# Optimization experiments

Measured on AMD Instinct MI355X. Metric: run time of the kernel, lower is better.

## Reference

```python
import jax, jax.numpy as jnp
import numpy as np

B, C, IMG, P, D, HEADS, L, DFF, NCLS = 32, 3, 384, 16, 512, 4, 6, 2048, 10
DH = D // HEADS          # 128
X = IMG // P             # 24 tokens per side
T = X * X                # 576 patch tokens
EPS = 1e-5               # torch LayerNorm default


def setup_inputs() -> dict:
    key = jax.random.key(0)
    ks = jax.random.split(key, 10)
    s = 0.02
    return {
        "img": jax.random.normal(ks[0], (B, C, IMG, IMG), jnp.float32),
        "Wpatch": jax.random.normal(ks[1], (C * P * P, D), jnp.float32) * s,
        "bpatch": jnp.zeros((D,), jnp.float32),
        "cls_token": jax.random.normal(ks[2], (1, 1, D), jnp.float32),
        "pos_emb": jax.random.normal(ks[3], (T + 1, D), jnp.float32),
        # per-layer params stacked on leading axis L for lax.scan
        "Wqkv": jax.random.normal(ks[4], (L, D, 3 * D), jnp.float32) * s,
        "W0": jax.random.normal(ks[5], (L, D, D), jnp.float32) * s,
        "g1": jnp.ones((L, D), jnp.float32), "b1": jnp.zeros((L, D), jnp.float32),
        "g2": jnp.ones((L, D), jnp.float32), "b2": jnp.zeros((L, D), jnp.float32),
        "W1": jax.random.normal(ks[6], (L, D, DFF), jnp.float32) * s,
        "bb1": jnp.zeros((L, DFF), jnp.float32),
        "W2": jax.random.normal(ks[7], (L, DFF, D), jnp.float32) * s,
        "bb2": jnp.zeros((L, D), jnp.float32),
        "Whead": jax.random.normal(ks[8], (D, NCLS), jnp.float32) * s,
        "bhead": jnp.zeros((NCLS,), jnp.float32),
    }


def _ln(x, g, b):
    m = x.mean(-1, keepdims=True)
    v = ((x - m) ** 2).mean(-1, keepdims=True)
    return (x - m) * jax.lax.rsqrt(v + EPS) * g + b


def _vit(img, Wpatch, bpatch, cls_token, pos_emb, Wqkv, W0,
         g1, b1, g2, b2, W1, bb1, W2, bb2, Whead, bhead):
    bsz = img.shape[0]
    # faithful rearrange 'b c (px x)(py y) -> b (x y)(px py c)' (strided patches)
    pat = img.reshape(bsz, C, P, X, P, X)            # (b, c, px, x, py, y)
    pat = pat.transpose(0, 3, 5, 2, 4, 1)            # (b, x, y, px, py, c)
    pat = pat.reshape(bsz, T, P * P * C)
    tok = pat @ Wpatch + bpatch                      # [b, T, D]
    tok = jnp.concatenate([jnp.broadcast_to(cls_token, (bsz, 1, D)), tok], axis=1)
    tok = tok + pos_emb[: T + 1]
    scale = DH ** -0.5

    def block(x, p):
        wqkv, w0, gg1, bg1, gg2, bg2, w1, c1, w2, c2 = p
        bt, tt, _ = x.shape
        # rearrange 'b t (d k h) -> k b h t d' with k=3
        qkv = (x @ wqkv).reshape(bt, tt, DH, 3, HEADS)
        q = qkv[..., 0, :].transpose(0, 3, 1, 2)     # [b, h, t, dh]
        k = qkv[..., 1, :].transpose(0, 3, 1, 2)
        v = qkv[..., 2, :].transpose(0, 3, 1, 2)
        attn = jax.nn.softmax(jnp.einsum('bhid,bhjd->bhij', q, k) * scale, axis=-1)
        o = jnp.einsum('bhij,bhjd->bhid', attn, v)
        o = o.transpose(0, 2, 1, 3).reshape(bt, tt, D) @ w0
        y = _ln(o + x, gg1, bg1)                     # postnorm block
        h = jax.nn.gelu(y @ w1 + c1, approximate=False) @ w2 + c2
        return _ln(h + y, gg2, bg2), None

    params = (Wqkv, W0, g1, b1, g2, b2, W1, bb1, W2, bb2)
    out, _ = jax.lax.scan(block, tok, params)
    return out[:, 0, :] @ Whead + bhead              # [b, NCLS]


def reference(img, Wpatch, bpatch, cls_token, pos_emb, Wqkv, W0,
              g1, b1, g2, b2, W1, bb1, W2, bb2, Whead, bhead):
    return _vit(img, Wpatch, bpatch, cls_token, pos_emb, Wqkv, W0,
                g1, b1, g2, b2, W1, bb1, W2, bb2, Whead, bhead)
```

## Files before the change

### kernel.cpp

```cpp
#include <hip/hip_runtime.h>
#include <hip/hip_bf16.h>


typedef unsigned short u16;
typedef __hip_bfloat16 bf16;
typedef __bf16 bf16x8 __attribute__((ext_vector_type(8)));
typedef float f32x4 __attribute__((ext_vector_type(4)));

typedef const __attribute__((address_space(1))) void* gas_ptr;
typedef __attribute__((address_space(3))) void* las_ptr;

#define TOKENS 577
#define TPAD   640
#define DMODEL 512
#define SM_SCALE 0.08838834764831845f
#define LAYER_W 3145728l

static __device__ __forceinline__ u16 f2b(float v) {
    bf16 t = __float2bfloat16(v);
    return *(u16*)&t;
}

template<int OUTMODE, bool GELU>
__global__ __launch_bounds__(256)
void gemm_bt(const u16* __restrict__ A, int lda,
             const u16* __restrict__ Bt, int ldb,
             float* __restrict__ Cf, bf16* __restrict__ Cb, int ldc,
             const float* __restrict__ bias, const float* __restrict__ pos,
             int K, int rows_valid)
{
    __shared__ u16 As[128 * 64];
    __shared__ u16 Bs[128 * 64];
    const int tid  = threadIdx.x;
    const int w    = tid >> 6;
    const int lane = tid & 63;
    const u16* Ab = A + (long)blockIdx.y * 128 * lda;
    const u16* Bb = Bt + (long)blockIdx.x * 128 * ldb;
    const int srow = w * 8 + (lane >> 3);
    const int scol = (lane & 7) * 8;
    const int wr = w >> 1, wc = w & 1;
    const int lr = lane & 15, lg = lane >> 4;
    f32x4 acc[4][4] = {};

    for (int kt = 0; kt < K; kt += 64) {
#pragma unroll
        for (int i = 0; i < 4; ++i) {
            const u16* ag = Ab + (long)(i * 32 + srow) * lda + kt + scol;
            const u16* bg = Bb + (long)(i * 32 + srow) * ldb + kt + scol;
            __builtin_amdgcn_global_load_lds((gas_ptr)ag, (las_ptr)&As[(i * 32 + w * 8) * 64], 16, 0, 0);
            __builtin_amdgcn_global_load_lds((gas_ptr)bg, (las_ptr)&Bs[(i * 32 + w * 8) * 64], 16, 0, 0);
        }
        __syncthreads();
#pragma unroll
        for (int kk = 0; kk < 2; ++kk) {
            const int ko = kk * 32 + lg * 8;
            bf16x8 af[4], bv[4];
#pragma unroll
            for (int m = 0; m < 4; ++m)
                af[m] = *(const bf16x8*)&As[(wr * 64 + m * 16 + lr) * 64 + ko];
#pragma unroll
            for (int n = 0; n < 4; ++n)
                bv[n] = *(const bf16x8*)&Bs[(wc * 64 + n * 16 + lr) * 64 + ko];
#pragma unroll
            for (int m = 0; m < 4; ++m)
#pragma unroll
                for (int n = 0; n < 4; ++n)
                    acc[m][n] = __builtin_amdgcn_mfma_f32_16x16x32_bf16(af[m], bv[n], acc[m][n], 0, 0, 0);
        }
        __syncthreads();
    }

    const int cbase = blockIdx.x * 128 + wc * 64;
    const int rbase = blockIdx.y * 128 + wr * 64;
#pragma unroll
    for (int n = 0; n < 4; ++n) {
        const int c = cbase + n * 16 + lr;
        const float bval = bias ? bias[c] : 0.0f;
#pragma unroll
        for (int m = 0; m < 4; ++m) {
#pragma unroll
            for (int j = 0; j < 4; ++j) {
                const int r = rbase + m * 16 + lg * 4 + j;
                if (r >= rows_valid) continue;
                float v = acc[m][n][j] + bval;
                if constexpr (GELU) v = 0.5f * v * (1.0f + erff(v * 0.70710678118654752f));
                long idx;
                if constexpr (OUTMODE == 1) {
                    const int pb = r / 576, pt = r - pb * 576;
                    v += pos[(long)(1 + pt) * DMODEL + c];
                    idx = (long)(pb * TOKENS + 1 + pt) * ldc + c;
                } else {
                    idx = (long)r * ldc + c;
                }
                if (Cf) Cf[idx] = v;
                if (Cb) Cb[idx] = __float2bfloat16(v);
            }
        }
    }
}

template<bool GELU, bool PACKED>
__global__ __launch_bounds__(256)
void gemm_bt32(const u16* __restrict__ A, int lda,
               const u16* __restrict__ Bt, int ldb,
               bf16* __restrict__ Cb, int ldc,
               const float* __restrict__ bias, int K, int rows_valid)
{
    __shared__ u16 As[128 * 32];
    __shared__ u16 Bs[128 * 32];
    const int tid  = threadIdx.x;
    const int w    = tid >> 6;
    const int lane = tid & 63;
    const u16* Ab = A + (long)blockIdx.y * 128 * lda;
    const u16* Bb = Bt + (long)blockIdx.x * 128 * ldb;
    const int wr = w >> 1, wc = w & 1;
    const int lr = lane & 15, lg = lane >> 4;
    f32x4 acc[4][4] = {};

    for (int kt = 0; kt < K; kt += 32) {
#pragma unroll
        for (int rd = 0; rd < 2; ++rd) {
            const int idx = rd * 256 + tid;
            const int row = idx >> 2, g = idx & 3;
            const int sg = g ^ ((row >> 1) & 3);
            __builtin_amdgcn_global_load_lds(
                (gas_ptr)(Ab + (long)row * lda + kt + sg * 8), (las_ptr)&As[idx * 8], 16, 0, 0);
            __builtin_amdgcn_global_load_lds(
                (gas_ptr)(Bb + (long)row * ldb + kt + sg * 8), (las_ptr)&Bs[idx * 8], 16, 0, 0);
        }
        __syncthreads();
        bf16x8 af[4], bv[4];
#pragma unroll
        for (int m = 0; m < 4; ++m) {
            const int r = wr * 64 + m * 16 + lr;
            af[m] = *(const bf16x8*)&As[r * 32 + (lg ^ ((r >> 1) & 3)) * 8];
        }
#pragma unroll
        for (int n = 0; n < 4; ++n) {
            const int r = wc * 64 + n * 16 + lr;
            bv[n] = *(const bf16x8*)&Bs[r * 32 + (lg ^ ((r >> 1) & 3)) * 8];
        }
#pragma unroll
        for (int m = 0; m < 4; ++m)
#pragma unroll
            for (int n = 0; n < 4; ++n)
                acc[m][n] = __builtin_amdgcn_mfma_f32_16x16x32_bf16(af[m], bv[n], acc[m][n], 0, 0, 0);
        __syncthreads();
    }

    const int cbase = blockIdx.x * 128 + wc * 64;
    const int rbase = blockIdx.y * 128 + wr * 64;
    float bval[4];
#pragma unroll
    for (int n = 0; n < 4; ++n) bval[n] = bias ? bias[cbase + n * 16 + lr] : 0.0f;

    if constexpr (PACKED) {
#pragma unroll
        for (int m = 0; m < 4; ++m) {
#pragma unroll
            for (int j = 0; j < 4; ++j) {
                const int r = rbase + m * 16 + lg * 4 + j;
                if (r >= rows_valid) continue;
                u16 pk[4];
#pragma unroll
                for (int n = 0; n < 4; ++n) {
                    float v = acc[m][n][j] + bval[n];
                    if constexpr (GELU) v = 0.5f * v * (1.0f + erff(v * 0.70710678118654752f));
                    pk[n] = f2b(v);
                }
                *(uint2*)&Cb[(long)r * ldc + cbase + lr * 4] = *(uint2*)pk;
            }
        }
    } else {
#pragma unroll
        for (int n = 0; n < 4; ++n) {
            const int c = cbase + n * 16 + lr;
#pragma unroll
            for (int m = 0; m < 4; ++m) {
#pragma unroll
                for (int j = 0; j < 4; ++j) {
                    const int r = rbase + m * 16 + lg * 4 + j;
                    if (r >= rows_valid) continue;
                    float v = acc[m][n][j] + bval[n];
                    if constexpr (GELU) v = 0.5f * v * (1.0f + erff(v * 0.70710678118654752f));
                    Cb[(long)r * ldc + c] = __float2bfloat16(v);
                }
            }
        }
    }
}

__global__ __launch_bounds__(512)
void proj_ln(const u16* __restrict__ A, const u16* __restrict__ Bt,
             const float* __restrict__ res,
             const float* __restrict__ g, const float* __restrict__ b,
             float* __restrict__ outf, bf16* __restrict__ outb, int Mrows)
{
    __shared__ u16 As[64 * 32];
    __shared__ u16 Bs[512 * 32];
    __shared__ float redS[4][64];
    __shared__ float redQ[4][64];
    const int tid = threadIdx.x, wid = tid >> 6, lane = tid & 63;
    const int wm = wid >> 2, wn = wid & 3;
    const int lr = lane & 15, lg = lane >> 4;
    const long row0 = (long)blockIdx.x * 64;
    const u16* Ab = A + row0 * DMODEL;
    f32x4 acc[2][8] = {};

    for (int kt = 0; kt < 512; kt += 32) {
#pragma unroll
        for (int rd = 0; rd < 4; ++rd) {
            const int idx = rd * 512 + tid;
            const int row = idx >> 2, gg = idx & 3;
            const int sg = gg ^ ((row >> 1) & 3);
            __builtin_amdgcn_global_load_lds(
                (gas_ptr)(Bt + (long)row * DMODEL + kt + sg * 8), (las_ptr)&Bs[idx * 8], 16, 0, 0);
        }
        if (tid < 256) {
            const int row = tid >> 2, gg = tid & 3;
            const int sg = gg ^ ((row >> 1) & 3);
            __builtin_amdgcn_global_load_lds(
                (gas_ptr)(Ab + (long)row * DMODEL + kt + sg * 8), (las_ptr)&As[tid * 8], 16, 0, 0);
        }
        __syncthreads();
        bf16x8 af[2], bv[8];
#pragma unroll
        for (int m = 0; m < 2; ++m) {
            const int r = wm * 32 + m * 16 + lr;
            af[m] = *(const bf16x8*)&As[r * 32 + (lg ^ ((r >> 1) & 3)) * 8];
        }
#pragma unroll
        for (int n = 0; n < 8; ++n) {
            const int r = wn * 128 + n * 16 + lr;
            bv[n] = *(const bf16x8*)&Bs[r * 32 + (lg ^ ((r >> 1) & 3)) * 8];
        }
#pragma unroll
        for (int m = 0; m < 2; ++m)
#pragma unroll
            for (int n = 0; n < 8; ++n)
                acc[m][n] = __builtin_amdgcn_mfma_f32_16x16x32_bf16(af[m], bv[n], acc[m][n], 0, 0, 0);
        __syncthreads();
    }

    float ps[2][4], pq[2][4];
#pragma unroll
    for (int m = 0; m < 2; ++m)
#pragma unroll
        for (int j = 0; j < 4; ++j) {
            const long r = row0 + wm * 32 + m * 16 + lg * 4 + j;
            const bool valid = r < Mrows;
            float s = 0.f, q = 0.f;
#pragma unroll
            for (int n = 0; n < 8; ++n) {
                float t = acc[m][n][j];
                if (valid) t += res[r * DMODEL + wn * 128 + n * 16 + lr];
                acc[m][n][j] = t;
                s += t; q += t * t;
            }
            ps[m][j] = s; pq[m][j] = q;
        }
#pragma unroll
    for (int o = 1; o < 16; o <<= 1)
#pragma unroll
        for (int m = 0; m < 2; ++m)
#pragma unroll
            for (int j = 0; j < 4; ++j) {
                ps[m][j] += __shfl_xor(ps[m][j], o);
                pq[m][j] += __shfl_xor(pq[m][j], o);
            }
    if (lr == 0) {
#pragma unroll
        for (int m = 0; m < 2; ++m)
#pragma unroll
            for (int j = 0; j < 4; ++j) {
                const int ri = wm * 32 + m * 16 + lg * 4 + j;
                redS[wn][ri] = ps[m][j];
                redQ[wn][ri] = pq[m][j];
            }
    }
    __syncthreads();
    if (tid < 64) {
        const float s = redS[0][tid] + redS[1][tid] + redS[2][tid] + redS[3][tid];
        const float q = redQ[0][tid] + redQ[1][tid] + redQ[2][tid] + redQ[3][tid];
        const float mean = s * (1.f / 512.f);
        const float var = q * (1.f / 512.f) - mean * mean;
        redS[0][tid] = mean;
        redQ[0][tid] = rsqrtf(var + 1e-5f);
    }
    __syncthreads();
#pragma unroll
    for (int m = 0; m < 2; ++m)
#pragma unroll
        for (int j = 0; j < 4; ++j) {
            const int ri = wm * 32 + m * 16 + lg * 4 + j;
            const long r = row0 + ri;
            if (r >= Mrows) continue;
            const float mean = redS[0][ri], rs = redQ[0][ri];
#pragma unroll
            for (int n = 0; n < 8; ++n) {
                const int c = wn * 128 + n * 16 + lr;
                const float o = (acc[m][n][j] - mean) * rs * g[c] + b[c];
                outf[r * DMODEL + c] = o;
                outb[r * DMODEL + c] = __float2bfloat16(o);
            }
        }
}

template<int OUTMODE, bool GELU>
__global__ __launch_bounds__(512, 1)
void gemm8(const u16* __restrict__ A, int lda,
           const u16* __restrict__ Bt, int ldb,
           float* __restrict__ Cf, bf16* __restrict__ Cb, int ldc,
           const float* __restrict__ bias, const float* __restrict__ pos,
           int K, int rows_valid)
{
    __shared__ u16 Ash[2][2][256 * 32];
    __shared__ u16 Bsh[2][2][256 * 32];
    const int tid = threadIdx.x, wid = tid >> 6, lane = tid & 63;
    const int wm = wid >> 2, wn = wid & 3;
    const int lr = lane & 15, lg = lane >> 4;
    const u16* Ab = A + (long)blockIdx.y * 256 * lda;
    const u16* Bb = Bt + (long)blockIdx.x * 256 * ldb;
    const int srow = tid >> 2;
    const int soct = ((tid & 3) ^ (srow & 3)) * 8;
    const int slot8 = (lg ^ (lr & 3)) * 8;

    f32x4 acc[8][4] = {};

    auto stage = [&](u16* dst, const u16* src, int ld, int kt, int kh) {
#pragma unroll
        for (int i = 0; i < 2; ++i)
            __builtin_amdgcn_global_load_lds(
                (gas_ptr)(src + (long)(i * 128 + srow) * ld + kt * 64 + kh * 32 + soct),
                (las_ptr)(dst + (i * 512 + tid) * 8), 16, 0, 0);
    };

#define VMW(n) { asm volatile("s_waitcnt vmcnt(" #n ")" ::: "memory"); \
                 __builtin_amdgcn_sched_barrier(0); }
#define MFMA16(A0)                                                              \
    __builtin_amdgcn_s_setprio(1);                                             \
    _Pragma("unroll")                                                           \
    for (int m = 0; m < 4; ++m)                                                 \
        _Pragma("unroll")                                                       \
        for (int n = 0; n < 4; ++n)                                             \
            acc[(A0) + m][n] = __builtin_amdgcn_mfma_f32_16x16x32_bf16(         \
                af[m], bfr[n], acc[(A0) + m][n], 0, 0, 0);                      \
    __builtin_amdgcn_s_setprio(0);

    const int nt = K / 64;
    stage(&Ash[0][0][0], Ab, lda, 0, 0);
    stage(&Bsh[0][0][0], Bb, ldb, 0, 0);
    stage(&Ash[0][1][0], Ab, lda, 0, 1);
    stage(&Bsh[0][1][0], Bb, ldb, 0, 1);
    VMW(4);
    __builtin_amdgcn_s_barrier();

    for (int t = 0; t < nt; ++t) {
        const int db = t & 1;
        const bool nx = (t + 1 < nt);
        bf16x8 af[4], bfr[4];

#pragma unroll
        for (int n = 0; n < 4; ++n)
            bfr[n] = *(const bf16x8*)&Bsh[db][0][(wn * 64 + n * 16 + lr) * 32 + slot8];
#pragma unroll
        for (int m = 0; m < 4; ++m)
            af[m] = *(const bf16x8*)&Ash[db][0][(wm * 128 + m * 16 + lr) * 32 + slot8];
        if (nx) stage(&Ash[db ^ 1][0][0], Ab, lda, t + 1, 0);
        __builtin_amdgcn_s_barrier();
        MFMA16(0)
        __builtin_amdgcn_s_barrier();

#pragma unroll
        for (int m = 0; m < 4; ++m)
            af[m] = *(const bf16x8*)&Ash[db][0][(wm * 128 + 64 + m * 16 + lr) * 32 + slot8];
        if (nx) { stage(&Bsh[db ^ 1][0][0], Bb, ldb, t + 1, 0); VMW(4); }
        else    { VMW(0); }
        __builtin_amdgcn_s_barrier();
        MFMA16(4)
        __builtin_amdgcn_s_barrier();

#pragma unroll
        for (int n = 0; n < 4; ++n)
            bfr[n] = *(const bf16x8*)&Bsh[db][1][(wn * 64 + n * 16 + lr) * 32 + slot8];
#pragma unroll
        for (int m = 0; m < 4; ++m)
            af[m] = *(const bf16x8*)&Ash[db][1][(wm * 128 + m * 16 + lr) * 32 + slot8];
        if (nx) stage(&Ash[db ^ 1][1][0], Ab, lda, t + 1, 1);
        __builtin_amdgcn_s_barrier();
        MFMA16(0)
        __builtin_amdgcn_s_barrier();

#pragma unroll
        for (int m = 0; m < 4; ++m)
            af[m] = *(const bf16x8*)&Ash[db][1][(wm * 128 + 64 + m * 16 + lr) * 32 + slot8];
        if (nx) { stage(&Bsh[db ^ 1][1][0], Bb, ldb, t + 1, 1); VMW(4); }
        __builtin_amdgcn_s_barrier();
        MFMA16(4)
        __builtin_amdgcn_s_barrier();
    }
#undef MFMA16
#undef VMW

    const int cbase = blockIdx.x * 256 + wn * 64;
    const int rbase = blockIdx.y * 256 + wm * 128;
#pragma unroll
    for (int n = 0; n < 4; ++n) {
        const int c = cbase + n * 16 + lr;
        const float bval = bias ? bias[c] : 0.0f;
#pragma unroll
        for (int a = 0; a < 8; ++a) {
#pragma unroll
            for (int j = 0; j < 4; ++j) {
                const int r = rbase + a * 16 + lg * 4 + j;
                if (r >= rows_valid) continue;
                float v = acc[a][n][j] + bval;
                if constexpr (GELU) v = 0.5f * v * (1.0f + erff(v * 0.70710678118654752f));
                long idx;
                if constexpr (OUTMODE == 1) {
                    const int pb = r / 576, pt = r - pb * 576;
                    v += pos[(long)(1 + pt) * DMODEL + c];
                    idx = (long)(pb * TOKENS + 1 + pt) * ldc + c;
                } else {
                    idx = (long)r * ldc + c;
                }
                if (Cf) Cf[idx] = v;
                if (Cb) Cb[idx] = __float2bfloat16(v);
            }
        }
    }
}

__global__ __launch_bounds__(256, 2)
void attn_flash(const u16* __restrict__ qkv, const u16* __restrict__ vhT,
                bf16* __restrict__ ob)
{
    __shared__ u16 Ksh[2][64 * 128];
    __shared__ u16 Vsh[2][128 * 64];
    __shared__ u16 Psh[128 * 64];
    const int tid = threadIdx.x;
    const int w = tid >> 6, lane = tid & 63;
    const int lr = lane & 15, lg = lane >> 4;
    const int pair = blockIdx.y;
    const int b = pair >> 2, h = pair & 3;
    const int q0 = blockIdx.x * 128;
    const long rowbase = (long)b * TOKENS;
    const int swrd = lr & 7;

    const u16* kg = qkv + rowbase * 1536 + 512 + h * 128;
    const u16* vg = vhT + (long)pair * 128 * TPAD;

    auto stageK = [&](int buf, int t) {
#pragma unroll
        for (int i = 0; i < 4; ++i) {
            const int slot = i * 256 + tid;
            const int row = slot >> 4, s = slot & 15;
            const int so = (s & 8) | ((s & 7) ^ (row & 7));
            __builtin_amdgcn_global_load_lds(
                (gas_ptr)(kg + (long)(t * 64 + row) * 1536 + so * 8),
                (las_ptr)&Ksh[buf][slot * 8], 16, 0, 0);
        }
    };
    auto stageV = [&](int buf, int t) {
#pragma unroll
        for (int i = 0; i < 4; ++i) {
            const int slot = i * 256 + tid;
            const int row = slot >> 3, s = slot & 7;
            const int so = s ^ (row & 7);
            __builtin_amdgcn_global_load_lds(
                (gas_ptr)(vg + (long)row * TPAD + t * 64 + so * 8),
                (las_ptr)&Vsh[buf][slot * 8], 16, 0, 0);
        }
    };

    bf16x8 qf[2][4];
#pragma unroll
    for (int m = 0; m < 2; ++m)
#pragma unroll
        for (int kf = 0; kf < 4; ++kf) {
            const long r = rowbase + q0 + w * 32 + m * 16 + lr;
            qf[m][kf] = *(const bf16x8*)&qkv[r * 1536 + h * 128 + kf * 32 + lg * 8];
        }

    float mrun[2][4], lrun[2][4];
#pragma unroll
    for (int m = 0; m < 2; ++m)
#pragma unroll
        for (int j = 0; j < 4; ++j) { mrun[m][j] = -1e30f; lrun[m][j] = 0.f; }
    f32x4 oacc[2][8] = {};

    constexpr int NT = TPAD / 64;
    stageK(0, 0); stageV(0, 0);
    stageK(1, 1); stageV(1, 1);
    asm volatile("s_waitcnt vmcnt(8)" ::: "memory");
    __builtin_amdgcn_sched_barrier(0);
    __builtin_amdgcn_s_barrier();

    for (int t = 0; t < NT; ++t) {
        const int cur = t & 1;

        f32x4 s[2][4] = {};
#pragma unroll
        for (int kf = 0; kf < 4; ++kf) {
            const int o = kf * 4 + lg;
            const int so = ((o & 8) | ((o & 7) ^ swrd)) * 8;
            bf16x8 bv[4];
#pragma unroll
            for (int n = 0; n < 4; ++n)
                bv[n] = *(const bf16x8*)&Ksh[cur][(n * 16 + lr) * 128 + so];
            __builtin_amdgcn_s_setprio(1);
#pragma unroll
            for (int m = 0; m < 2; ++m)
#pragma unroll
                for (int n = 0; n < 4; ++n)
                    s[m][n] = __builtin_amdgcn_mfma_f32_16x16x32_bf16(qf[m][kf], bv[n], s[m][n], 0, 0, 0);
            __builtin_amdgcn_s_setprio(0);
        }

        float sc[2][4];
#pragma unroll
        for (int m = 0; m < 2; ++m)
#pragma unroll
            for (int jj = 0; jj < 4; ++jj) {
                float mx = mrun[m][jj];
#pragma unroll
                for (int n = 0; n < 4; ++n) {
                    const int col = t * 64 + n * 16 + lr;
                    float v = s[m][n][jj] * SM_SCALE;
                    v = (col < TOKENS) ? v : -1e30f;
                    s[m][n][jj] = v;
                    mx = fmaxf(mx, v);
                }
#pragma unroll
                for (int o = 1; o < 16; o <<= 1) mx = fmaxf(mx, __shfl_xor(mx, o));
                const float f = __expf(mrun[m][jj] - mx);
                sc[m][jj] = f;
                float sum = 0.f;
#pragma unroll
                for (int n = 0; n < 4; ++n) {
                    const float p = __expf(s[m][n][jj] - mx);
                    s[m][n][jj] = p;
                    sum += p;
                }
#pragma unroll
                for (int o = 1; o < 16; o <<= 1) sum += __shfl_xor(sum, o);
                lrun[m][jj] = lrun[m][jj] * f + sum;
                mrun[m][jj] = mx;
            }
#pragma unroll
        for (int m = 0; m < 2; ++m)
#pragma unroll
            for (int n = 0; n < 8; ++n)
#pragma unroll
                for (int jj = 0; jj < 4; ++jj) oacc[m][n][jj] *= sc[m][jj];

#pragma unroll
        for (int m = 0; m < 2; ++m)
#pragma unroll
            for (int jj = 0; jj < 4; ++jj) {
                const int prow = w * 32 + m * 16 + lg * 4 + jj;
                const int p7 = prow & 7;
#pragma unroll
                for (int n = 0; n < 4; ++n) {
                    const int c = n * 16 + lr;
                    Psh[prow * 64 + (((c >> 3) ^ p7) << 3) + (c & 7)] = f2b(s[m][n][jj]);
                }
            }

#pragma unroll
        for (int kf = 0; kf < 2; ++kf) {
            const int so = ((kf * 4 + lg) ^ swrd) * 8;
            bf16x8 pa[2];
#pragma unroll
            for (int m = 0; m < 2; ++m)
                pa[m] = *(const bf16x8*)&Psh[(w * 32 + m * 16 + lr) * 64 + so];
            __builtin_amdgcn_s_setprio(1);
#pragma unroll
            for (int n = 0; n < 8; ++n) {
                const bf16x8 vb = *(const bf16x8*)&Vsh[cur][(n * 16 + lr) * 64 + so];
#pragma unroll
                for (int m = 0; m < 2; ++m)
                    oacc[m][n] = __builtin_amdgcn_mfma_f32_16x16x32_bf16(pa[m], vb, oacc[m][n], 0, 0, 0);
            }
            __builtin_amdgcn_s_setprio(0);
        }

        __builtin_amdgcn_s_barrier();
        if (t + 2 < NT) { stageK(cur, t + 2); stageV(cur, t + 2); }
        if (t + 1 < NT) {
            if (t + 2 < NT) { asm volatile("s_waitcnt vmcnt(8)" ::: "memory"); }
            else            { asm volatile("s_waitcnt vmcnt(0)" ::: "memory"); }
            __builtin_amdgcn_sched_barrier(0);
        }
        __builtin_amdgcn_s_barrier();
    }

#pragma unroll
    for (int m = 0; m < 2; ++m)
#pragma unroll
        for (int jj = 0; jj < 4; ++jj) {
            const float inv = 1.f / lrun[m][jj];
            const int q = q0 + w * 32 + m * 16 + lg * 4 + jj;
            if (q >= TOKENS) continue;
#pragma unroll
            for (int n = 0; n < 8; ++n)
                ob[(rowbase + q) * DMODEL + h * 128 + n * 16 + lr] =
                    __float2bfloat16(oacc[m][n][jj] * inv);
        }
}

__global__ __launch_bounds__(256)
void wtrans(const float* __restrict__ W, bf16* __restrict__ WT, int K, int N)
{
    __shared__ float tile[32][33];
    const int n0 = blockIdx.x * 32, k0 = blockIdx.y * 32;
    const int tx = threadIdx.x & 31, ty = threadIdx.x >> 5;
#pragma unroll
    for (int i = 0; i < 4; ++i)
        tile[ty + i * 8][tx] = W[(long)(k0 + ty + i * 8) * N + n0 + tx];
    __syncthreads();
#pragma unroll
    for (int i = 0; i < 4; ++i)
        WT[(long)(n0 + ty + i * 8) * K + k0 + tx] = __float2bfloat16(tile[tx][ty + i * 8]);
}

__global__ __launch_bounds__(256)
void wtrans_layers(const float* __restrict__ Wqkv, const float* __restrict__ W0,
                   const float* __restrict__ W1, const float* __restrict__ W2,
                   bf16* __restrict__ out, int layer0)
{
    const int bb = blockIdx.x;
    const int sl = bb / 3072;
    const int l = layer0 + sl;
    int t = bb % 3072;
    bf16* base = out + (long)sl * LAYER_W;
    const float* W; bf16* WT; int K, N; int mode = 0;
    if (t < 768)       {            W = Wqkv + (long)l * 512 * 1536; WT = base;           K = 512;  N = 1536; mode = 1; }
    else if (t < 1024) { t -= 768;  W = W0   + (long)l * 512 * 512;  WT = base + 786432;  K = 512;  N = 512;  }
    else if (t < 2048) { t -= 1024; W = W1   + (long)l * 512 * 2048; WT = base + 1048576; K = 512;  N = 2048; }
    else               { t -= 2048; W = W2   + (long)l * 2048 * 512; WT = base + 2097152; K = 2048; N = 512;  mode = 2; }
    const int nx = N / 32;
    const int n0 = (t % nx) * 32, k0 = (t / nx) * 32;
    __shared__ float tile[32][33];
    const int tx = threadIdx.x & 31, ty = threadIdx.x >> 5;
#pragma unroll
    for (int i = 0; i < 4; ++i)
        tile[ty + i * 8][tx] = W[(long)(k0 + ty + i * 8) * N + n0 + tx];
    __syncthreads();
#pragma unroll
    for (int i = 0; i < 4; ++i) {
        int n = n0 + ty + i * 8;
        if (mode == 1) {
            const int d = n / 12, rr = n % 12;
            n = (rr >> 2) * 512 + (rr & 3) * 128 + d;
        }
        int kk = k0 + tx;
        if (mode == 2) {
            const int s = kk & 63;
            kk = (kk & ~63) | (((s & 15) << 2) | (s >> 4));
        }
        WT[(long)n * K + kk] = __float2bfloat16(tile[tx][ty + i * 8]);
    }
}

__global__ __launch_bounds__(64)
void patch_gather(const float* __restrict__ img, bf16* __restrict__ pat)
{
    const int bid = blockIdx.x;
    const int x  = bid % 24;
    const int p1 = (bid / 24) % 16;
    const int b  = bid / (24 * 16);
    __shared__ bf16 lds[24][48];
    const int lane = threadIdx.x;
    const int h = p1 * 24 + x;
    for (int c = 0; c < 3; ++c) {
        const float* row = img + ((long)(b * 3 + c) * 384 + h) * 384;
#pragma unroll
        for (int i = 0; i < 6; ++i) {
            const int wpix = lane + i * 64;
            const float v = row[wpix];
            const int y = wpix % 24, p2 = wpix / 24;
            lds[y][p2 * 3 + c] = __float2bfloat16(v);
        }
    }
    __syncthreads();
    for (int idx = lane; idx < 24 * 48; idx += 64) {
        const int y = idx / 48, j = idx % 48;
        pat[(long)(b * 576 + x * 24 + y) * 768 + p1 * 48 + j] = lds[y][j];
    }
}

__global__ __launch_bounds__(256)
void clsfill(const float* __restrict__ cls, const float* __restrict__ pos,
             float* __restrict__ tokf, bf16* __restrict__ xb)
{
    const int i = blockIdx.x * 256 + threadIdx.x;
    const int b = i >> 9, d = i & 511;
    const float v = cls[d] + pos[d];
    tokf[(long)b * TOKENS * DMODEL + d] = v;
    xb[(long)b * TOKENS * DMODEL + d] = __float2bfloat16(v);
}

__global__ __launch_bounds__(256)
void repack_v(const u16* __restrict__ qkv, u16* __restrict__ vhT)
{
    __shared__ u16 lds[64][136];
    const int bid = blockIdx.x;
    const int tt = bid % 10, pair = bid / 10;
    const int b = pair >> 2, h = pair & 3;
    const int tid = threadIdx.x;
    const int tl = tid >> 2, seg = tid & 3;
    const long row = (long)b * TOKENS + tt * 64 + tl;
    const u16* src = qkv + row * 1536 + 1024 + h * 128 + seg * 32;
#pragma unroll
    for (int u = 0; u < 4; ++u)
        *(uint4*)&lds[tl][seg * 32 + u * 8] = *(const uint4*)&src[u * 8];
    __syncthreads();
    const int d = tid >> 1, th = (tid & 1) * 32;
    u16* dst = vhT + ((long)pair * 128 + d) * TPAD + tt * 64 + th;
#pragma unroll
    for (int blk = 0; blk < 4; ++blk) {
        uint4 pk; u16* pp = (u16*)&pk;
#pragma unroll
        for (int j = 0; j < 8; ++j) {
            const int t = tt * 64 + th + blk * 8 + j;
            pp[j] = (t < TOKENS) ? lds[th + blk * 8 + j][d] : (u16)0;
        }
        *(uint4*)&dst[blk * 8] = pk;
    }
}

__global__ __launch_bounds__(256)
void resln(const float* __restrict__ xin, const float* __restrict__ res,
           const float* __restrict__ g, const float* __restrict__ b,
           float* __restrict__ outf, bf16* __restrict__ outb, int nrows)
{
    const int row = blockIdx.x * 4 + (threadIdx.x >> 6);
    if (row >= nrows) return;
    const int lane = threadIdx.x & 63;
    const float* p1 = xin + (long)row * DMODEL;
    const float* p2 = res + (long)row * DMODEL;
    float v[8];
    float s = 0.f;
#pragma unroll
    for (int i = 0; i < 8; ++i) { v[i] = p1[lane + i * 64] + p2[lane + i * 64]; s += v[i]; }
#pragma unroll
    for (int o = 32; o; o >>= 1) s += __shfl_xor(s, o);
    const float mean = s * (1.f / 512.f);
    float q = 0.f;
#pragma unroll
    for (int i = 0; i < 8; ++i) { const float d = v[i] - mean; q += d * d; }
#pragma unroll
    for (int o = 32; o; o >>= 1) q += __shfl_xor(q, o);
    const float rs = rsqrtf(q * (1.f / 512.f) + 1e-5f);
#pragma unroll
    for (int i = 0; i < 8; ++i) {
        const int c = lane + i * 64;
        const float o = (v[i] - mean) * rs * g[c] + b[c];
        outf[(long)row * DMODEL + c] = o;
        outb[(long)row * DMODEL + c] = __float2bfloat16(o);
    }
}

__global__ __launch_bounds__(64)
void head_k(const float* __restrict__ tokf, const float* __restrict__ Wh,
            const float* __restrict__ bh, float* __restrict__ out)
{
    const int b = blockIdx.x;
    const int lane = threadIdx.x;
    const float* x = tokf + (long)b * TOKENS * DMODEL;
    float acc[10] = {};
#pragma unroll
    for (int i = 0; i < 8; ++i) {
        const int d = lane + i * 64;
        const float xv = x[d];
        const float* wr = Wh + (long)d * 10;
#pragma unroll
        for (int c = 0; c < 10; ++c) acc[c] += xv * wr[c];
    }
#pragma unroll
    for (int c = 0; c < 10; ++c)
#pragma unroll
        for (int o = 32; o; o >>= 1) acc[c] += __shfl_xor(acc[c], o);
    if (lane == 0) {
#pragma unroll
        for (int c = 0; c < 10; ++c) out[b * 10 + c] = acc[c] + bh[c];
    }
}

extern "C" void kernel_launch(void* const* d_in, const int* in_sizes, int n_in,
                              void* d_out, int out_size, void* d_ws, size_t ws_size,
                              hipStream_t stream)
{
    (void)in_sizes; (void)n_in; (void)out_size;
    const float* img    = (const float*)d_in[0];
    const float* Wpatch = (const float*)d_in[1];
    const float* bpatch = (const float*)d_in[2];
    const float* clstk  = (const float*)d_in[3];
    const float* pos    = (const float*)d_in[4];
    const float* Wqkv   = (const float*)d_in[5];
    const float* W0     = (const float*)d_in[6];
    const float* g1     = (const float*)d_in[7];
    const float* b1     = (const float*)d_in[8];
    const float* g2     = (const float*)d_in[9];
    const float* b2     = (const float*)d_in[10];
    const float* W1     = (const float*)d_in[11];
    const float* bb1    = (const float*)d_in[12];
    const float* W2     = (const float*)d_in[13];
    const float* bb2    = (const float*)d_in[14];
    const float* Whead  = (const float*)d_in[15];
    const float* bhead  = (const float*)d_in[16];

    static const int cand[7][2] = {{32,6},{32,1},{16,1},{8,1},{4,1},{2,1},{1,1}};
    int Bc = 0, nW = 1;
    size_t o_tokf=0, o_xb=0, o_R1=0, o_R2=0, o_ob=0, o_wp=0, o_wr=0;
    for (int ci = 0; ci < 7; ++ci) {
        const int bc = cand[ci][0], nw = cand[ci][1];
        const long Mrows = (long)bc * TOKENS;
        const long Mpad  = ((Mrows + 255) / 256) * 256;
        size_t off = 0;
        auto take = [&](size_t sz) { size_t o = off; off += (sz + 255) & ~(size_t)255; return o; };
        size_t t_tokf = take((size_t)Mpad * 512 * 4);
        size_t t_xb   = take((size_t)Mpad * 512 * 2);
        size_t t_R1   = take((size_t)Mpad * 2048 * 2);
        size_t r2a = (size_t)bc * 4 * TPAD * 128 * 2;
        size_t r2b = (size_t)Mpad * 512 * 4;
        size_t t_R2 = take(r2a > r2b ? r2a : r2b);
        size_t t_ob   = take((size_t)Mpad * 512 * 2);
        size_t t_wp   = take((size_t)512 * 768 * 2);
        size_t t_wr   = take((size_t)nw * LAYER_W * 2);
        if (off <= ws_size) {
            Bc = bc; nW = nw;
            o_tokf=t_tokf; o_xb=t_xb; o_R1=t_R1; o_R2=t_R2; o_ob=t_ob; o_wp=t_wp; o_wr=t_wr;
            break;
        }
    }
    if (Bc == 0) return;

    const long Mrows = (long)Bc * TOKENS;
    const long Mpad  = ((Mrows + 255) / 256) * 256;
    const int  NP    = Bc * 4;
    const int  gy128 = (int)(Mpad / 128);
    const int  gy256 = (int)(Mpad / 256);
    const int  nproj = (int)((Mrows + 63) / 64);
    const long patRows = ((long)Bc * 576 + 127) / 128 * 128;

    char* base = (char*)d_ws;
    float* tokf = (float*)(base + o_tokf);
    bf16*  xb   = (bf16*)(base + o_xb);
    char*  R1   = base + o_R1;
    char*  R2   = base + o_R2;
    bf16*  ob   = (bf16*)(base + o_ob);
    bf16*  wpT  = (bf16*)(base + o_wp);
    bf16*  wAll = (bf16*)(base + o_wr);

    u16*  qkvb = (u16*)R1;
    bf16* pat  = (bf16*)R1;
    u16*  h1b  = (u16*)R1;
    u16*  vhT  = (u16*)R2;
    float* t1  = (float*)R2;

    wtrans<<<dim3(512 / 32, 768 / 32), 256, 0, stream>>>(Wpatch, wpT, 768, 512);
    if (nW == 6)
        wtrans_layers<<<6 * 3072, 256, 0, stream>>>(Wqkv, W0, W1, W2, wAll, 0);

    const int nchunks = 32 / Bc;
    for (int ch = 0; ch < nchunks; ++ch) {
        const float* img_c = img + (long)ch * Bc * 3 * 384 * 384;

        hipMemsetAsync(xb, 0, (size_t)Mpad * 512 * 2, stream);
        clsfill<<<Bc * 2, 256, 0, stream>>>(clstk, pos, tokf, xb);
        patch_gather<<<Bc * 16 * 24, 64, 0, stream>>>(img_c, pat);
        gemm_bt<1, false><<<dim3(4, (int)(patRows / 128)), 256, 0, stream>>>(
            (const u16*)pat, 768, (const u16*)wpT, 768,
            tokf, xb, 512, bpatch, pos, 768, Bc * 576);

        for (int l = 0; l < 6; ++l) {
            const bf16* wL = wAll + (nW == 6 ? (long)l * LAYER_W : 0);
            if (nW == 1)
                wtrans_layers<<<3072, 256, 0, stream>>>(Wqkv, W0, W1, W2, wAll, l);
            const u16* wqkvT = (const u16*)wL;
            const u16* w0T   = (const u16*)(wL + 786432);
            const u16* w1T   = (const u16*)(wL + 1048576);
            const u16* w2T   = (const u16*)(wL + 2097152);

            gemm_bt32<false, false><<<dim3(12, gy128), 256, 0, stream>>>(
                (const u16*)xb, 512, wqkvT, 512,
                (bf16*)qkvb, 1536, nullptr, 512, (int)Mpad);

            repack_v<<<NP * 10, 256, 0, stream>>>(qkvb, vhT);
            attn_flash<<<dim3(5, NP), 256, 0, stream>>>(qkvb, vhT, ob);

            proj_ln<<<nproj, 512, 0, stream>>>(
                (const u16*)ob, w0T, tokf, g1 + l * 512, b1 + l * 512,
                tokf, xb, (int)Mrows);

            gemm_bt32<true, true><<<dim3(16, gy128), 256, 0, stream>>>(
                (const u16*)xb, 512, w1T, 512,
                (bf16*)h1b, 2048, bb1 + l * 2048, 512, (int)Mrows);

            gemm8<0, false><<<dim3(2, gy256), 512, 0, stream>>>(
                (const u16*)h1b, 2048, w2T, 2048,
                t1, nullptr, 512, bb2 + l * 512, nullptr, 2048, (int)Mrows);
            resln<<<(int)((Mrows + 3) / 4), 256, 0, stream>>>(
                t1, tokf, g2 + l * 512, b2 + l * 512, tokf, xb, (int)Mrows);
        }

        head_k<<<Bc, 64, 0, stream>>>(tokf, Whead, bhead, (float*)d_out + (long)ch * Bc * 10);
    }
}
```

Before: 2.646 ms.

## Replace custom FFN2 and patch GEMMs with shared 128-tile kernel and bf16 output

New measurement: 2.448 ms. 1.08x faster.

```diff
diff --git a/kernel.cpp b/kernel.cpp
--- a/kernel.cpp
+++ b/kernel.cpp
@@ -21,90 +21,13 @@
     return *(u16*)&t;
 }
 
-template<int OUTMODE, bool GELU>
-__global__ __launch_bounds__(256)
-void gemm_bt(const u16* __restrict__ A, int lda,
-             const u16* __restrict__ Bt, int ldb,
-             float* __restrict__ Cf, bf16* __restrict__ Cb, int ldc,
-             const float* __restrict__ bias, const float* __restrict__ pos,
-             int K, int rows_valid)
-{
-    __shared__ u16 As[128 * 64];
-    __shared__ u16 Bs[128 * 64];
-    const int tid  = threadIdx.x;
-    const int w    = tid >> 6;
-    const int lane = tid & 63;
-    const u16* Ab = A + (long)blockIdx.y * 128 * lda;
-    const u16* Bb = Bt + (long)blockIdx.x * 128 * ldb;
-    const int srow = w * 8 + (lane >> 3);
-    const int scol = (lane & 7) * 8;
-    const int wr = w >> 1, wc = w & 1;
-    const int lr = lane & 15, lg = lane >> 4;
-    f32x4 acc[4][4] = {};
-
-    for (int kt = 0; kt < K; kt += 64) {
-#pragma unroll
-        for (int i = 0; i < 4; ++i) {
-            const u16* ag = Ab + (long)(i * 32 + srow) * lda + kt + scol;
-            const u16* bg = Bb + (long)(i * 32 + srow) * ldb + kt + scol;
-            __builtin_amdgcn_global_load_lds((gas_ptr)ag, (las_ptr)&As[(i * 32 + w * 8) * 64], 16, 0, 0);
-            __builtin_amdgcn_global_load_lds((gas_ptr)bg, (las_ptr)&Bs[(i * 32 + w * 8) * 64], 16, 0, 0);
-        }
-        __syncthreads();
-#pragma unroll
-        for (int kk = 0; kk < 2; ++kk) {
-            const int ko = kk * 32 + lg * 8;
-            bf16x8 af[4], bv[4];
-#pragma unroll
-            for (int m = 0; m < 4; ++m)
-                af[m] = *(const bf16x8*)&As[(wr * 64 + m * 16 + lr) * 64 + ko];
-#pragma unroll
-            for (int n = 0; n < 4; ++n)
-                bv[n] = *(const bf16x8*)&Bs[(wc * 64 + n * 16 + lr) * 64 + ko];
-#pragma unroll
-            for (int m = 0; m < 4; ++m)
-#pragma unroll
-                for (int n = 0; n < 4; ++n)
-                    acc[m][n] = __builtin_amdgcn_mfma_f32_16x16x32_bf16(af[m], bv[n], acc[m][n], 0, 0, 0);
-        }
-        __syncthreads();
-    }
-
-    const int cbase = blockIdx.x * 128 + wc * 64;
-    const int rbase = blockIdx.y * 128 + wr * 64;
-#pragma unroll
-    for (int n = 0; n < 4; ++n) {
-        const int c = cbase + n * 16 + lr;
-        const float bval = bias ? bias[c] : 0.0f;
-#pragma unroll
-        for (int m = 0; m < 4; ++m) {
-#pragma unroll
-            for (int j = 0; j < 4; ++j) {
-                const int r = rbase + m * 16 + lg * 4 + j;
-                if (r >= rows_valid) continue;
-                float v = acc[m][n][j] + bval;
-                if constexpr (GELU) v = 0.5f * v * (1.0f + erff(v * 0.70710678118654752f));
-                long idx;
-                if constexpr (OUTMODE == 1) {
-                    const int pb = r / 576, pt = r - pb * 576;
-                    v += pos[(long)(1 + pt) * DMODEL + c];
-                    idx = (long)(pb * TOKENS + 1 + pt) * ldc + c;
-                } else {
-                    idx = (long)r * ldc + c;
-                }
-                if (Cf) Cf[idx] = v;
-                if (Cb) Cb[idx] = __float2bfloat16(v);
-            }
-        }
-    }
-}
-
-template<bool GELU, bool PACKED>
+template<bool GELU, int OMODE>
 __global__ __launch_bounds__(256)
 void gemm_bt32(const u16* __restrict__ A, int lda,
                const u16* __restrict__ Bt, int ldb,
-               bf16* __restrict__ Cb, int ldc,
-               const float* __restrict__ bias, int K, int rows_valid)
+               bf16* __restrict__ Cb, float* __restrict__ Cf, int ldc,
+               const float* __restrict__ bias, const float* __restrict__ pos,
+               int K, int rows_valid)
 {
     __shared__ u16 As[128 * 32];
     __shared__ u16 Bs[128 * 32];
@@ -154,7 +77,7 @@
 #pragma unroll
     for (int n = 0; n < 4; ++n) bval[n] = bias ? bias[cbase + n * 16 + lr] : 0.0f;
 
-    if constexpr (PACKED) {
+    if constexpr (OMODE == 1) {
 #pragma unroll
         for (int m = 0; m < 4; ++m) {
 #pragma unroll
@@ -169,6 +92,24 @@
                     pk[n] = f2b(v);
                 }
                 *(uint2*)&Cb[(long)r * ldc + cbase + lr * 4] = *(uint2*)pk;
+            }
+        }
+    } else if constexpr (OMODE == 3) {
+#pragma unroll
+        for (int m = 0; m < 4; ++m) {
+#pragma unroll
+            for (int j = 0; j < 4; ++j) {
+                const int r = rbase + m * 16 + lg * 4 + j;
+                if (r >= rows_valid) continue;
+                const int pb = r / 576, pt = r - pb * 576;
+                const long orow = (long)pb * TOKENS + 1 + pt;
+#pragma unroll
+                for (int n = 0; n < 4; ++n) {
+                    const int c = cbase + n * 16 + lr;
+                    const float v = acc[m][n][j] + bval[n] + pos[(long)(1 + pt) * DMODEL + c];
+                    Cf[orow * ldc + c] = v;
+                    Cb[orow * ldc + c] = __float2bfloat16(v);
+                }
             }
         }
     } else {
@@ -304,131 +245,6 @@
                 outb[r * DMODEL + c] = __float2bfloat16(o);
             }
         }
-}
-
-template<int OUTMODE, bool GELU>
-__global__ __launch_bounds__(512, 1)
-void gemm8(const u16* __restrict__ A, int lda,
-           const u16* __restrict__ Bt, int ldb,
-           float* __restrict__ Cf, bf16* __restrict__ Cb, int ldc,
-           const float* __restrict__ bias, const float* __restrict__ pos,
-           int K, int rows_valid)
-{
-    __shared__ u16 Ash[2][2][256 * 32];
-    __shared__ u16 Bsh[2][2][256 * 32];
-    const int tid = threadIdx.x, wid = tid >> 6, lane = tid & 63;
-    const int wm = wid >> 2, wn = wid & 3;
-    const int lr = lane & 15, lg = lane >> 4;
-    const u16* Ab = A + (long)blockIdx.y * 256 * lda;
-    const u16* Bb = Bt + (long)blockIdx.x * 256 * ldb;
-    const int srow = tid >> 2;
-    const int soct = ((tid & 3) ^ (srow & 3)) * 8;
-    const int slot8 = (lg ^ (lr & 3)) * 8;
-
-    f32x4 acc[8][4] = {};
-
-    auto stage = [&](u16* dst, const u16* src, int ld, int kt, int kh) {
-#pragma unroll
-        for (int i = 0; i < 2; ++i)
-            __builtin_amdgcn_global_load_lds(
-                (gas_ptr)(src + (long)(i * 128 + srow) * ld + kt * 64 + kh * 32 + soct),
-                (las_ptr)(dst + (i * 512 + tid) * 8), 16, 0, 0);
-    };
-
-#define VMW(n) { asm volatile("s_waitcnt vmcnt(" #n ")" ::: "memory"); \
-                 __builtin_amdgcn_sched_barrier(0); }
-#define MFMA16(A0)                                                              \
-    __builtin_amdgcn_s_setprio(1);                                             \
-    _Pragma("unroll")                                                           \
-    for (int m = 0; m < 4; ++m)                                                 \
-        _Pragma("unroll")                                                       \
-        for (int n = 0; n < 4; ++n)                                             \
-            acc[(A0) + m][n] = __builtin_amdgcn_mfma_f32_16x16x32_bf16(         \
-                af[m], bfr[n], acc[(A0) + m][n], 0, 0, 0);                      \
-    __builtin_amdgcn_s_setprio(0);
-
-    const int nt = K / 64;
-    stage(&Ash[0][0][0], Ab, lda, 0, 0);
-    stage(&Bsh[0][0][0], Bb, ldb, 0, 0);
-    stage(&Ash[0][1][0], Ab, lda, 0, 1);
-    stage(&Bsh[0][1][0], Bb, ldb, 0, 1);
-    VMW(4);
-    __builtin_amdgcn_s_barrier();
-
-    for (int t = 0; t < nt; ++t) {
-        const int db = t & 1;
-        const bool nx = (t + 1 < nt);
-        bf16x8 af[4], bfr[4];
-
-#pragma unroll
-        for (int n = 0; n < 4; ++n)
-            bfr[n] = *(const bf16x8*)&Bsh[db][0][(wn * 64 + n * 16 + lr) * 32 + slot8];
-#pragma unroll
-        for (int m = 0; m < 4; ++m)
-            af[m] = *(const bf16x8*)&Ash[db][0][(wm * 128 + m * 16 + lr) * 32 + slot8];
-        if (nx) stage(&Ash[db ^ 1][0][0], Ab, lda, t + 1, 0);
-        __builtin_amdgcn_s_barrier();
-        MFMA16(0)
-        __builtin_amdgcn_s_barrier();
-
-#pragma unroll
-        for (int m = 0; m < 4; ++m)
-            af[m] = *(const bf16x8*)&Ash[db][0][(wm * 128 + 64 + m * 16 + lr) * 32 + slot8];
-        if (nx) { stage(&Bsh[db ^ 1][0][0], Bb, ldb, t + 1, 0); VMW(4); }
-        else    { VMW(0); }
-        __builtin_amdgcn_s_barrier();
-        MFMA16(4)
-        __builtin_amdgcn_s_barrier();
-
-#pragma unroll
-        for (int n = 0; n < 4; ++n)
-            bfr[n] = *(const bf16x8*)&Bsh[db][1][(wn * 64 + n * 16 + lr) * 32 + slot8];
-#pragma unroll
-        for (int m = 0; m < 4; ++m)
-            af[m] = *(const bf16x8*)&Ash[db][1][(wm * 128 + m * 16 + lr) * 32 + slot8];
-        if (nx) stage(&Ash[db ^ 1][1][0], Ab, lda, t + 1, 1);
-        __builtin_amdgcn_s_barrier();
-        MFMA16(0)
-        __builtin_amdgcn_s_barrier();
-
-#pragma unroll
-        for (int m = 0; m < 4; ++m)
-            af[m] = *(const bf16x8*)&Ash[db][1][(wm * 128 + 64 + m * 16 + lr) * 32 + slot8];
-        if (nx) { stage(&Bsh[db ^ 1][1][0], Bb, ldb, t + 1, 1); VMW(4); }
-        __builtin_amdgcn_s_barrier();
-        MFMA16(4)
-        __builtin_amdgcn_s_barrier();
-    }
-#undef MFMA16
-#undef VMW
-
-    const int cbase = blockIdx.x * 256 + wn * 64;
-    const int rbase = blockIdx.y * 256 + wm * 128;
-#pragma unroll
-    for (int n = 0; n < 4; ++n) {
-        const int c = cbase + n * 16 + lr;
-        const float bval = bias ? bias[c] : 0.0f;
-#pragma unroll
-        for (int a = 0; a < 8; ++a) {
-#pragma unroll
-            for (int j = 0; j < 4; ++j) {
-                const int r = rbase + a * 16 + lg * 4 + j;
-                if (r >= rows_valid) continue;
-                float v = acc[a][n][j] + bval;
-                if constexpr (GELU) v = 0.5f * v * (1.0f + erff(v * 0.70710678118654752f));
-                long idx;
-                if constexpr (OUTMODE == 1) {
-                    const int pb = r / 576, pt = r - pb * 576;
-                    v += pos[(long)(1 + pt) * DMODEL + c];
-                    idx = (long)(pb * TOKENS + 1 + pt) * ldc + c;
-                } else {
-                    idx = (long)r * ldc + c;
-                }
-                if (Cf) Cf[idx] = v;
-                if (Cb) Cb[idx] = __float2bfloat16(v);
-            }
-        }
-    }
 }
 
 __global__ __launch_bounds__(256, 2)
@@ -636,7 +452,7 @@
     bf16* base = out + (long)sl * LAYER_W;
     const float* W; bf16* WT; int K, N; int mode = 0;
     if (t < 768)       {            W = Wqkv + (long)l * 512 * 1536; WT = base;           K = 512;  N = 1536; mode = 1; }
-    else if (t < 1024) { t -= 768;  W = W0   + (long)l * 512 * 512;  WT = base + 786432;  K = 512;  N = 512;  }
+    else if (t < 1024) { t -= 768;  W = W0   + (long)l * 512 * 512;  WT = base + 786432;  K = 512;  N = 512;  mode = 2; }
     else if (t < 2048) { t -= 1024; W = W1   + (long)l * 512 * 2048; WT = base + 1048576; K = 512;  N = 2048; }
     else               { t -= 2048; W = W2   + (long)l * 2048 * 512; WT = base + 2097152; K = 2048; N = 512;  mode = 2; }
     const int nx = N / 32;
@@ -731,19 +547,22 @@
 }
 
 __global__ __launch_bounds__(256)
-void resln(const float* __restrict__ xin, const float* __restrict__ res,
+void resln(const bf16* __restrict__ xin, const float* __restrict__ res,
            const float* __restrict__ g, const float* __restrict__ b,
            float* __restrict__ outf, bf16* __restrict__ outb, int nrows)
 {
     const int row = blockIdx.x * 4 + (threadIdx.x >> 6);
     if (row >= nrows) return;
     const int lane = threadIdx.x & 63;
-    const float* p1 = xin + (long)row * DMODEL;
+    const bf16* p1 = xin + (long)row * DMODEL;
     const float* p2 = res + (long)row * DMODEL;
     float v[8];
     float s = 0.f;
 #pragma unroll
-    for (int i = 0; i < 8; ++i) { v[i] = p1[lane + i * 64] + p2[lane + i * 64]; s += v[i]; }
+    for (int i = 0; i < 8; ++i) {
+        v[i] = __bfloat162float(p1[lane + i * 64]) + p2[lane + i * 64];
+        s += v[i];
+    }
 #pragma unroll
     for (int o = 32; o; o >>= 1) s += __shfl_xor(s, o);
     const float mean = s * (1.f / 512.f);
@@ -817,14 +636,14 @@
     for (int ci = 0; ci < 7; ++ci) {
         const int bc = cand[ci][0], nw = cand[ci][1];
         const long Mrows = (long)bc * TOKENS;
-        const long Mpad  = ((Mrows + 255) / 256) * 256;
+        const long Mpad  = ((Mrows + 127) / 128) * 128;
         size_t off = 0;
         auto take = [&](size_t sz) { size_t o = off; off += (sz + 255) & ~(size_t)255; return o; };
         size_t t_tokf = take((size_t)Mpad * 512 * 4);
         size_t t_xb   = take((size_t)Mpad * 512 * 2);
         size_t t_R1   = take((size_t)Mpad * 2048 * 2);
         size_t r2a = (size_t)bc * 4 * TPAD * 128 * 2;
-        size_t r2b = (size_t)Mpad * 512 * 4;
+        size_t r2b = (size_t)Mpad * 512 * 2;
         size_t t_R2 = take(r2a > r2b ? r2a : r2b);
         size_t t_ob   = take((size_t)Mpad * 512 * 2);
         size_t t_wp   = take((size_t)512 * 768 * 2);
@@ -838,12 +657,11 @@
     if (Bc == 0) return;
 
     const long Mrows = (long)Bc * TOKENS;
-    const long Mpad  = ((Mrows + 255) / 256) * 256;
+    const long Mpad  = ((Mrows + 127) / 128) * 128;
     const int  NP    = Bc * 4;
     const int  gy128 = (int)(Mpad / 128);
-    const int  gy256 = (int)(Mpad / 256);
     const int  nproj = (int)((Mrows + 63) / 64);
-    const long patRows = ((long)Bc * 576 + 127) / 128 * 128;
+    const int  gyp   = (int)(((long)Bc * 576 + 127) / 128);
 
     char* base = (char*)d_ws;
     float* tokf = (float*)(base + o_tokf);
@@ -858,7 +676,7 @@
     bf16* pat  = (bf16*)R1;
     u16*  h1b  = (u16*)R1;
     u16*  vhT  = (u16*)R2;
-    float* t1  = (float*)R2;
+    bf16* t1b  = (bf16*)R2;
 
     wtrans<<<dim3(512 / 32, 768 / 32), 256, 0, stream>>>(Wpatch, wpT, 768, 512);
     if (nW == 6)
@@ -871,9 +689,9 @@
         hipMemsetAsync(xb, 0, (size_t)Mpad * 512 * 2, stream);
         clsfill<<<Bc * 2, 256, 0, stream>>>(clstk, pos, tokf, xb);
         patch_gather<<<Bc * 16 * 24, 64, 0, stream>>>(img_c, pat);
-        gemm_bt<1, false><<<dim3(4, (int)(patRows / 128)), 256, 0, stream>>>(
+        gemm_bt32<false, 3><<<dim3(4, gyp), 256, 0, stream>>>(
             (const u16*)pat, 768, (const u16*)wpT, 768,
-            tokf, xb, 512, bpatch, pos, 768, Bc * 576);
+            xb, tokf, 512, bpatch, pos, 768, Bc * 576);
 
         for (int l = 0; l < 6; ++l) {
             const bf16* wL = wAll + (nW == 6 ? (long)l * LAYER_W : 0);
@@ -884,9 +702,9 @@
             const u16* w1T   = (const u16*)(wL + 1048576);
             const u16* w2T   = (const u16*)(wL + 2097152);
 
-            gemm_bt32<false, false><<<dim3(12, gy128), 256, 0, stream>>>(
+            gemm_bt32<false, 1><<<dim3(12, gy128), 256, 0, stream>>>(
                 (const u16*)xb, 512, wqkvT, 512,
-                (bf16*)qkvb, 1536, nullptr, 512, (int)Mpad);
+                (bf16*)qkvb, nullptr, 1536, nullptr, nullptr, 512, (int)Mpad);
 
             repack_v<<<NP * 10, 256, 0, stream>>>(qkvb, vhT);
             attn_flash<<<dim3(5, NP), 256, 0, stream>>>(qkvb, vhT, ob);
@@ -895,15 +713,16 @@
                 (const u16*)ob, w0T, tokf, g1 + l * 512, b1 + l * 512,
                 tokf, xb, (int)Mrows);
 
-            gemm_bt32<true, true><<<dim3(16, gy128), 256, 0, stream>>>(
+            gemm_bt32<true, 1><<<dim3(16, gy128), 256, 0, stream>>>(
                 (const u16*)xb, 512, w1T, 512,
-                (bf16*)h1b, 2048, bb1 + l * 2048, 512, (int)Mrows);
-
-            gemm8<0, false><<<dim3(2, gy256), 512, 0, stream>>>(
+                (bf16*)h1b, nullptr, 2048, bb1 + l * 2048, nullptr, 512, (int)Mrows);
+
+            gemm_bt32<false, 0><<<dim3(4, gy128), 256, 0, stream>>>(
                 (const u16*)h1b, 2048, w2T, 2048,
-                t1, nullptr, 512, bb2 + l * 512, nullptr, 2048, (int)Mrows);
+                t1b, nullptr, 512, bb2 + l * 512, nullptr, 2048, (int)Mrows);
+
             resln<<<(int)((Mrows + 3) / 4), 256, 0, stream>>>(
-                t1, tokf, g2 + l * 512, b2 + l * 512, tokf, xb, (int)Mrows);
+                t1b, tokf, g2 + l * 512, b2 + l * 512, tokf, xb, (int)Mrows);
         }
 
         head_k<<<Bc, 64, 0, stream>>>(tokf, Whead, bhead, (float*)d_out + (long)ch * Bc * 10);
```
